# Optimization experiments

Hardware: AMD Instinct MI355X
Metric: run time of the kernel (lower is better)

The kernel has to match this reference:

```python
import jax, jax.numpy as jnp
import numpy as np

EMB = 1024
HEADS = 16
HD = EMB // HEADS

def setup_inputs() -> dict:
    key = jax.random.key(0)
    ks = jax.random.split(key, 9)
    s = 1.0 / np.sqrt(EMB)
    x = jax.random.normal(ks[0], (4, 2048, EMB), dtype=jnp.float32)
    Wq = jax.random.uniform(ks[1], (EMB, EMB), jnp.float32, -s, s)
    bq = jax.random.uniform(ks[2], (EMB,), jnp.float32, -s, s)
    Wk = jax.random.uniform(ks[3], (EMB, EMB), jnp.float32, -s, s)
    bk = jax.random.uniform(ks[4], (EMB,), jnp.float32, -s, s)
    Wv = jax.random.uniform(ks[5], (EMB, EMB), jnp.float32, -s, s)
    bv = jax.random.uniform(ks[6], (EMB,), jnp.float32, -s, s)
    Wo = jax.random.uniform(ks[7], (EMB, EMB), jnp.float32, -s, s)
    bo = jax.random.uniform(ks[8], (EMB,), jnp.float32, -s, s)
    return {"x": x, "Wq": Wq, "bq": bq, "Wk": Wk, "bk": bk, "Wv": Wv, "bv": bv, "Wo": Wo, "bo": bo}

def reference(x, Wq, bq, Wk, bk, Wv, bv, Wo, bo):
    B, T, C = x.shape
    # projections (torch Linear: y = x @ W^T + b)
    q = (x @ Wq.T + bq).reshape(B, T, HEADS, HD).transpose(0, 2, 1, 3)  # [B,H,T,hd]
    k = (x @ Wk.T + bk).reshape(B, T, HEADS, HD).transpose(0, 2, 1, 3)
    v = (x @ Wv.T + bv).reshape(B, T, HEADS, HD).transpose(0, 2, 1, 3)
    scores = jnp.einsum('bhqd,bhkd->bhqk', q, k) / jnp.sqrt(jnp.float32(HD))
    weights = jax.nn.softmax(scores, axis=-1)
    attn = jnp.einsum('bhqk,bhkd->bhqd', weights, v)
    out = attn.transpose(0, 2, 1, 3).reshape(B, T, C)
    return out @ Wo.T + bo
```

## Files before the change

### kernel.cpp

```cpp
#include <hip/hip_runtime.h>

#define TSEQ  2048
#define BATCH 4
#define NHEAD 16
#define EMB   1024

typedef __attribute__((ext_vector_type(8))) __bf16 bf16x8;
typedef __attribute__((ext_vector_type(4))) __bf16 bf16x4;
typedef __attribute__((ext_vector_type(4))) float  floatx4;
typedef __attribute__((ext_vector_type(2))) unsigned int uint32x2;
typedef __attribute__((ext_vector_type(4))) unsigned int uint32x4;

__device__ __forceinline__ void gload_lds16(const __bf16* g, __bf16* lds_uniform_base) {
  __builtin_amdgcn_global_load_lds(
      (__attribute__((address_space(1))) void*)(g),
      (__attribute__((address_space(3))) void*)(lds_uniform_base),
      16, 0, 0);
}

__global__ __launch_bounds__(256) void cvt_f32_bf16(
    const float* __restrict__ src, __bf16* __restrict__ dst)
{
  const int gid = (blockIdx.x * 256 + threadIdx.x) * 4;
  const float4 v = *(const float4*)(src + gid);
  dst[gid + 0] = (__bf16)v.x;
  dst[gid + 1] = (__bf16)v.y;
  dst[gid + 2] = (__bf16)v.z;
  dst[gid + 3] = (__bf16)v.w;
}

__global__ __launch_bounds__(256) void cvt_w4(
    const float* __restrict__ s0, const float* __restrict__ s1,
    const float* __restrict__ s2, const float* __restrict__ s3,
    __bf16* __restrict__ d0, __bf16* __restrict__ d1,
    __bf16* __restrict__ d2, __bf16* __restrict__ d3)
{
  const int z = blockIdx.z;
  const float* src = (z == 0) ? s0 : (z == 1) ? s1 : (z == 2) ? s2 : s3;
  __bf16*      dst = (z == 0) ? d0 : (z == 1) ? d1 : (z == 2) ? d2 : d3;
  const int gid = (blockIdx.x * 256 + threadIdx.x) * 4;
  const float4 v = *(const float4*)(src + gid);
  dst[gid + 0] = (__bf16)v.x;
  dst[gid + 1] = (__bf16)v.y;
  dst[gid + 2] = (__bf16)v.z;
  dst[gid + 3] = (__bf16)v.w;
}

#define GK_NT 16

#define GEMM_STAGE(BUF, K0)                                                               \
  {                                                                                       \
    _Pragma("unroll")                                                                     \
    for (int c = 0; c < 4; c++) {                                                         \
      gload_lds16(aStage + (size_t)(c * 32) * 1024 + (K0),                                \
                  &As[BUF][(c * 32 + wid * 8) * 64]);                                     \
      gload_lds16(bStage + (size_t)(c * 32) * 1024 + (K0),                                \
                  &Bs[BUF][(c * 32 + wid * 8) * 64]);                                     \
    }                                                                                     \
  }

#define GEMM_BODY(C_STORE)                                                                \
  const int tid  = threadIdx.x;                                                           \
  const int lane = tid & 63;                                                              \
  const int wid  = tid >> 6;                                                              \
  const int l16  = lane & 15;                                                             \
  const int quad = lane >> 4;                                                             \
  const int wm   = wid & 1;                                                               \
  const int wn   = wid >> 1;                                                              \
  const int lin = blockIdx.x + blockIdx.y * 8;                                            \
  const int swz = (lin & 7) * 64 + (lin >> 3);                                            \
  const int m0  = (swz >> 3) * 128;                                                       \
  const int n0  = (swz & 7) * 128;                                                        \
  __shared__ alignas(16) __bf16 As[2][128 * 64];                                          \
  __shared__ alignas(16) __bf16 Bs[2][128 * 64];                                          \
  floatx4 acc[4][4];                                                                      \
  _Pragma("unroll")                                                                       \
  for (int i = 0; i < 4; i++)                                                             \
    _Pragma("unroll")                                                                     \
    for (int j = 0; j < 4; j++) acc[i][j] = (floatx4){0.f, 0.f, 0.f, 0.f};                \
  const int lrow = lane >> 3;                                                             \
  const int xsg  = (lane & 7) ^ lrow;                                                     \
  const __bf16* aStage = A + (size_t)(m0 + wid * 8 + lrow) * 1024 + xsg * 8;              \
  const __bf16* bStage = W + (size_t)(n0 + wid * 8 + lrow) * 1024 + xsg * 8;              \
  const int h7 = l16 & 7;                                                                 \
  GEMM_STAGE(0, 0)                                                                        \
  GEMM_STAGE(1, 64)                                                                       \
  __asm__ __volatile__("s_waitcnt vmcnt(8)\n\ts_barrier" ::: "memory");                   \
  int cur = 0;                                                                            \
  _Pragma("unroll 1")                                                                     \
  for (int k = 0; k < GK_NT; ++k) {                                                       \
    bf16x8 af0[4], af1[4], bf0[4], bf1[4];                                                \
    _Pragma("unroll")                                                                     \
    for (int i = 0; i < 4; i++) {                                                         \
      const int ar = (wm * 64 + i * 16 + l16) * 64;                                       \
      const int br = (wn * 64 + i * 16 + l16) * 64;                                       \
      af0[i] = *(const bf16x8*)(&As[cur][ar + ((quad ^ h7)) * 8]);                        \
      af1[i] = *(const bf16x8*)(&As[cur][ar + (((4 + quad) ^ h7)) * 8]);                  \
      bf0[i] = *(const bf16x8*)(&Bs[cur][br + ((quad ^ h7)) * 8]);                        \
      bf1[i] = *(const bf16x8*)(&Bs[cur][br + (((4 + quad) ^ h7)) * 8]);                  \
    }                                                                                     \
    _Pragma("unroll")                                                                     \
    for (int i = 0; i < 4; i++)                                                           \
      _Pragma("unroll")                                                                   \
      for (int j = 0; j < 4; j++) {                                                       \
        acc[i][j] = __builtin_amdgcn_mfma_f32_16x16x32_bf16(af0[i], bf0[j], acc[i][j], 0, 0, 0); \
        acc[i][j] = __builtin_amdgcn_mfma_f32_16x16x32_bf16(af1[i], bf1[j], acc[i][j], 0, 0, 0); \
      }                                                                                   \
    __asm__ __volatile__("s_waitcnt lgkmcnt(0)\n\ts_barrier" ::: "memory");               \
    if (k < GK_NT - 2) {                                                                  \
      GEMM_STAGE(cur, (k + 2) * 64)                                                       \
      __asm__ __volatile__("s_waitcnt vmcnt(8)\n\ts_barrier" ::: "memory");               \
    } else if (k == GK_NT - 2) {                                                          \
      __asm__ __volatile__("s_waitcnt vmcnt(0)\n\ts_barrier" ::: "memory");               \
    }                                                                                     \
    cur ^= 1;                                                                             \
  }                                                                                       \
  float bv[4];                                                                            \
  _Pragma("unroll")                                                                       \
  for (int j = 0; j < 4; j++) bv[j] = Bb[n0 + wn * 64 + j * 16 + l16];                    \
  _Pragma("unroll")                                                                       \
  for (int i = 0; i < 4; i++) {                                                           \
    const size_t mrow = (size_t)m0 + wm * 64 + i * 16 + quad * 4;                         \
    _Pragma("unroll")                                                                     \
    for (int j = 0; j < 4; j++) {                                                         \
      const int col = n0 + wn * 64 + j * 16 + l16;                                        \
      _Pragma("unroll")                                                                   \
      for (int r = 0; r < 4; r++) C_STORE;                                                \
    }                                                                                     \
  }

__global__ __launch_bounds__(256) void gemm_bt_bias(
    const __bf16* __restrict__ A,
    const __bf16* __restrict__ W0, const __bf16* __restrict__ W1, const __bf16* __restrict__ W2,
    const float* __restrict__ B0, const float* __restrict__ B1, const float* __restrict__ B2,
    __bf16* __restrict__ C0, __bf16* __restrict__ C1, __bf16* __restrict__ C2)
{
  const int z = blockIdx.z;
  const __bf16* W  = (z == 0) ? W0 : ((z == 1) ? W1 : W2);
  const float*  Bb = (z == 0) ? B0 : ((z == 1) ? B1 : B2);
  __bf16*       C  = (z == 0) ? C0 : ((z == 1) ? C1 : C2);
  const float  scl = (z == 0) ? 0.125f * 1.44269504088896340736f : 1.0f;
  GEMM_BODY(C[(mrow + r) * 1024 + col] = (__bf16)((acc[i][j][r] + bv[j]) * scl))
}

__global__ __launch_bounds__(256) void gemm_bt_bias_f32(
    const __bf16* __restrict__ A, const __bf16* __restrict__ W,
    const float* __restrict__ Bb, float* __restrict__ C)
{
  GEMM_BODY(C[(mrow + r) * 1024 + col] = acc[i][j][r] + bv[j])
}

__global__ __launch_bounds__(256) void v_transpose(
    const __bf16* __restrict__ V, __bf16* __restrict__ VT)
{
  const int t0 = blockIdx.x * 64;
  const int bh = blockIdx.y;
  const int b  = bh >> 4;
  const int h  = bh & 15;
  const int tid = threadIdx.x;

  __shared__ alignas(16) __bf16 Ls[64 * 72];

  const int row = tid >> 2, seg = tid & 3;
  const __bf16* src = V + ((size_t)(b * TSEQ + t0 + row)) * EMB + h * 64;
  *(bf16x8*)(&Ls[row * 72 + seg * 8])       = *(const bf16x8*)(src + seg * 8);
  *(bf16x8*)(&Ls[row * 72 + (seg + 4) * 8]) = *(const bf16x8*)(src + (seg + 4) * 8);
  __syncthreads();

  const int od = tid >> 2, oseg = tid & 3;
  bf16x8 o0, o1;
#pragma unroll
  for (int j = 0; j < 8; j++) o0[j] = Ls[(oseg * 16 + j) * 72 + od];
#pragma unroll
  for (int j = 0; j < 8; j++) o1[j] = Ls[(oseg * 16 + 8 + j) * 72 + od];
  __bf16* dst = VT + ((size_t)bh * 64 + od) * TSEQ + t0 + oseg * 16;
  *(bf16x8*)(dst)     = o0;
  *(bf16x8*)(dst + 8) = o1;
}

#define KVB 64
#define NT  (TSEQ / KVB)

#define FA_ZERO (floatx4){0.f, 0.f, 0.f, 0.f}

#define FA_STAGE(BUF, TILE)                                                               \
  if ((TILE) < NT) {                                                                      \
    _Pragma("unroll")                                                                     \
    for (int c = 0; c < 2; c++) {                                                         \
      gload_lds16(kstage + (size_t)((TILE) * KVB + c * 8) * EMB,                          \
                  &Ks[BUF][(wid * 16 + c * 8) * 64]);                                     \
      gload_lds16(vstage + (size_t)(c * 8) * TSEQ + (TILE) * KVB,                         \
                  &VTs[BUF][(wid * 16 + c * 8) * 64]);                                    \
    }                                                                                     \
  }

#define SM_PACK(TA, TB, DST)                                                              \
  {                                                                                       \
    bf16x4 pa_, pb_;                                                                      \
    _Pragma("unroll")                                                                     \
    for (int r = 0; r < 4; r++) pa_[r] = (__bf16)__builtin_amdgcn_exp2f((TA)[r]);         \
    _Pragma("unroll")                                                                     \
    for (int r = 0; r < 4; r++) pb_[r] = (__bf16)__builtin_amdgcn_exp2f((TB)[r]);         \
    const uint32x2 A2_ = __builtin_bit_cast(uint32x2, pa_);                               \
    const uint32x2 B2_ = __builtin_bit_cast(uint32x2, pb_);                               \
    const uint32x2 r0_ = __builtin_amdgcn_permlane32_swap(A2_.x, B2_.x, false, false);    \
    const uint32x2 r1_ = __builtin_amdgcn_permlane32_swap(A2_.y, B2_.y, false, false);    \
    const uint32x2 s0_ = __builtin_amdgcn_permlane16_swap(r0_.x, r0_.y, false, false);    \
    const uint32x2 s1_ = __builtin_amdgcn_permlane16_swap(r1_.x, r1_.y, false, false);    \
    const uint32x4 fw_ = (uint32x4){s0_.x, s1_.x, s0_.y, s1_.y};                          \
    DST = __builtin_bit_cast(bf16x8, fw_);                                                \
  }

#define QK_BLOCK(BUF, KS, TA, TB)                                                         \
  {                                                                                       \
    const bf16x8 ka0 = *(const bf16x8*)(&Ks[BUF][(KS) * 2048 + aoff0]);                   \
    const bf16x8 ka1 = *(const bf16x8*)(&Ks[BUF][(KS) * 2048 + aoff1]);                   \
    const bf16x8 kb0 = *(const bf16x8*)(&Ks[BUF][(KS) * 2048 + 1024 + aoff0]);            \
    const bf16x8 kb1 = *(const bf16x8*)(&Ks[BUF][(KS) * 2048 + 1024 + aoff1]);            \
    _Pragma("unroll")                                                                     \
    for (int g = 0; g < 2; g++) {                                                         \
      TA[g] = FA_ZERO;                                                                    \
      TA[g] = __builtin_amdgcn_mfma_f32_16x16x32_bf16(ka0, qf[g][0], TA[g], 0, 0, 0);     \
      TA[g] = __builtin_amdgcn_mfma_f32_16x16x32_bf16(ka1, qf[g][1], TA[g], 0, 0, 0);     \
      TB[g] = FA_ZERO;                                                                    \
      TB[g] = __builtin_amdgcn_mfma_f32_16x16x32_bf16(kb0, qf[g][0], TB[g], 0, 0, 0);     \
      TB[g] = __builtin_amdgcn_mfma_f32_16x16x32_bf16(kb1, qf[g][1], TB[g], 0, 0, 0);     \
    }                                                                                     \
  }

#define FA_STEP(BUF, KT)                                                                  \
  {                                                                                       \
    __builtin_amdgcn_s_setprio(1);                                                        \
    floatx4 ta[2], tb[2];                                                                 \
    QK_BLOCK(BUF, 0, ta, tb)                                                              \
    _Pragma("unroll")                                                                     \
    for (int g = 0; g < 2; g++) {                                                         \
      bf16x8 nf;                                                                          \
      SM_PACK(ta[g], tb[g], nf)                                                           \
      _Pragma("unroll")                                                                   \
      for (int dg = 0; dg < 4; dg++) {                                                    \
        const bf16x8 v0 = *(const bf16x8*)(&VTs[(BUF) ^ 1][dg * 1024 + aoff0]);           \
        Oacc[g][dg] = __builtin_amdgcn_mfma_f32_16x16x32_bf16(v0, pfragP[g][0], Oacc[g][dg], 0, 0, 0); \
      }                                                                                   \
      lacc[g] = __builtin_amdgcn_mfma_f32_16x16x32_bf16(ones, pfragP[g][0], lacc[g], 0, 0, 0); \
      _Pragma("unroll")                                                                   \
      for (int dg = 0; dg < 4; dg++) {                                                    \
        const bf16x8 v1 = *(const bf16x8*)(&VTs[(BUF) ^ 1][dg * 1024 + aoff1]);           \
        Oacc[g][dg] = __builtin_amdgcn_mfma_f32_16x16x32_bf16(v1, pfragP[g][1], Oacc[g][dg], 0, 0, 0); \
      }                                                                                   \
      lacc[g] = __builtin_amdgcn_mfma_f32_16x16x32_bf16(ones, pfragP[g][1], lacc[g], 0, 0, 0); \
      pfragP[g][0] = nf;                                                                  \
    }                                                                                     \
    QK_BLOCK(BUF, 1, ta, tb)                                                              \
    __builtin_amdgcn_s_setprio(0);                                                        \
    __syncthreads();                                                                      \
    FA_STAGE((BUF) ^ 1, (KT) + 1);                                                        \
    _Pragma("unroll")                                                                     \
    for (int g = 0; g < 2; g++) { SM_PACK(ta[g], tb[g], pfragP[g][1]) }                   \
    __syncthreads();                                                                      \
  }

__global__ __launch_bounds__(256, 2) void flash_attn(
    const __bf16* __restrict__ Q, const __bf16* __restrict__ K,
    const __bf16* __restrict__ VT, __bf16* __restrict__ O)
{
  const int lin = blockIdx.x + blockIdx.y * 16;
  const int swz = (lin & 7) * 128 + (lin >> 3);
  const int qt  = swz & 15;
  const int bh  = swz >> 4;
  const int b    = bh >> 4;
  const int h    = bh & 15;
  const int tid  = threadIdx.x;
  const int wid  = tid >> 6;
  const int lane = tid & 63;
  const int l16  = lane & 15;
  const int quad = lane >> 4;

  __shared__ alignas(16) __bf16 Ks[2][KVB * 64];
  __shared__ alignas(16) __bf16 VTs[2][64 * 64];

  const size_t base = ((size_t)b * TSEQ) * EMB + (size_t)h * 64;
  const __bf16* qptr  = Q + base;
  const __bf16* kptr  = K + base;
  const __bf16* vtptr = VT + (size_t)bh * 64 * TSEQ;
  __bf16*       optr  = O + base;

  const int qb = qt * 128 + wid * 32;

  bf16x8 qf[2][2];
#pragma unroll
  for (int g = 0; g < 2; g++)
#pragma unroll
    for (int hf = 0; hf < 2; hf++)
      qf[g][hf] = *(const bf16x8*)(qptr + (size_t)(qb + g * 16 + l16) * EMB + hf * 32 + quad * 8);

  floatx4 Oacc[2][4];
#pragma unroll
  for (int g = 0; g < 2; g++)
#pragma unroll
    for (int dg = 0; dg < 4; dg++) Oacc[g][dg] = FA_ZERO;
  floatx4 lacc[2];
#pragma unroll
  for (int g = 0; g < 2; g++) lacc[g] = FA_ZERO;

  const uint32x4 onesw = (uint32x4){0x3F803F80u, 0x3F803F80u, 0x3F803F80u, 0x3F803F80u};
  const bf16x8 ones = __builtin_bit_cast(bf16x8, onesw);

  const int lrow = lane >> 3;
  const int xsg  = (lane & 7) ^ lrow;
  const __bf16* kstage = kptr  + (size_t)(wid * 16 + lrow) * EMB  + xsg * 8;
  const __bf16* vstage = vtptr + (size_t)(wid * 16 + lrow) * TSEQ + xsg * 8;

  const int h7    = l16 & 7;
  const int x0    = quad ^ h7;
  const int aoff0 = l16 * 64 + x0 * 8;
  const int aoff1 = l16 * 64 + (x0 ^ 4) * 8;

  bf16x8 pfragP[2][2];

  FA_STAGE(0, 0);
  __syncthreads();
  FA_STAGE(1, 1);
  {
    floatx4 ta[2], tb[2];
    QK_BLOCK(0, 0, ta, tb)
#pragma unroll
    for (int g = 0; g < 2; g++) { SM_PACK(ta[g], tb[g], pfragP[g][0]) }
    QK_BLOCK(0, 1, ta, tb)
#pragma unroll
    for (int g = 0; g < 2; g++) { SM_PACK(ta[g], tb[g], pfragP[g][1]) }
  }
  __syncthreads();

#pragma unroll 1
  for (int kt = 1; kt < NT - 1; kt += 2) {
    FA_STEP(1, kt);
    FA_STEP(0, kt + 1);
  }
  FA_STEP(1, NT - 1);

#pragma unroll
  for (int g = 0; g < 2; g++) {
#pragma unroll
    for (int dg = 0; dg < 4; dg++) {
      const bf16x8 v0 = *(const bf16x8*)(&VTs[1][dg * 1024 + aoff0]);
      const bf16x8 v1 = *(const bf16x8*)(&VTs[1][dg * 1024 + aoff1]);
      Oacc[g][dg] = __builtin_amdgcn_mfma_f32_16x16x32_bf16(v0, pfragP[g][0], Oacc[g][dg], 0, 0, 0);
      Oacc[g][dg] = __builtin_amdgcn_mfma_f32_16x16x32_bf16(v1, pfragP[g][1], Oacc[g][dg], 0, 0, 0);
    }
    lacc[g] = __builtin_amdgcn_mfma_f32_16x16x32_bf16(ones, pfragP[g][0], lacc[g], 0, 0, 0);
    lacc[g] = __builtin_amdgcn_mfma_f32_16x16x32_bf16(ones, pfragP[g][1], lacc[g], 0, 0, 0);
  }

#pragma unroll
  for (int g = 0; g < 2; g++) {
    const float inv = 1.0f / lacc[g][0];
#pragma unroll
    for (int dg = 0; dg < 4; dg++) {
      bf16x4 ov;
#pragma unroll
      for (int r = 0; r < 4; r++) ov[r] = (__bf16)(Oacc[g][dg][r] * inv);
      *(bf16x4*)(optr + (size_t)(qb + g * 16 + l16) * EMB + dg * 16 + quad * 4) = ov;
    }
  }
}

extern "C" void kernel_launch(void* const* d_in, const int* in_sizes, int n_in,
                              void* d_out, int out_size, void* d_ws, size_t ws_size,
                              hipStream_t stream) {
  const float* x  = (const float*)d_in[0];
  const float* Wq = (const float*)d_in[1];
  const float* bq = (const float*)d_in[2];
  const float* Wk = (const float*)d_in[3];
  const float* bk = (const float*)d_in[4];
  const float* Wv = (const float*)d_in[5];
  const float* bv = (const float*)d_in[6];
  const float* Wo = (const float*)d_in[7];
  const float* bo = (const float*)d_in[8];
  float* out = (float*)d_out;

  const size_t NELEM = (size_t)BATCH * TSEQ * EMB;
  const size_t WELEM = (size_t)EMB * EMB;

  __bf16* q_b  = (__bf16*)d_out;
  __bf16* k_b  = q_b + NELEM;
  __bf16* x_b  = (__bf16*)d_ws;
  __bf16* v_b  = x_b + NELEM;
  __bf16* wq_b = v_b + NELEM;
  __bf16* wk_b = wq_b + WELEM;
  __bf16* wv_b = wk_b + WELEM;
  __bf16* wo_b = wv_b + WELEM;

  dim3 blk(256, 1, 1);

  cvt_f32_bf16<<<(int)(NELEM / 1024), blk, 0, stream>>>(x, x_b);
  cvt_w4<<<dim3((int)(WELEM / 1024), 1, 4), blk, 0, stream>>>(
      Wq, Wk, Wv, Wo, wq_b, wk_b, wv_b, wo_b);

  gemm_bt_bias<<<dim3(8, 64, 3), blk, 0, stream>>>(
      x_b, wq_b, wk_b, wv_b, bq, bk, bv, q_b, k_b, v_b);

  v_transpose<<<dim3(TSEQ / 64, BATCH * NHEAD), blk, 0, stream>>>(v_b, x_b);

  flash_attn<<<dim3(TSEQ / 128, BATCH * NHEAD), blk, 0, stream>>>(
      q_b, k_b, x_b, v_b);

  gemm_bt_bias_f32<<<dim3(8, 64, 1), blk, 0, stream>>>(v_b, wo_b, bo, out);
}
```

Measured before the change: 265.9 us.

## Enlarge GEMM tiles to 256x128 with 8 waves and double flash-attn query tile

The projection GEMMs move to 512-thread blocks computing 256x128 output tiles. Fragment loads and MFMAs are interleaved in four quadrant phases, with setprio around the MFMAs and barriers between phases, and the next-stage prefetch is issued mid-iteration. Flash attention now processes 256 query rows per block (64 per wave) and hoists the V fragment loads out of the per-group loop, so each K/V tile is reused across more queries. This is meant to cut global/LDS traffic per FLOP and improve MFMA issue density, at the cost of higher register pressure and fewer blocks in the grid.

```diff
diff --git a/kernel.cpp b/kernel.cpp
--- a/kernel.cpp
+++ b/kernel.cpp
@@ -46,32 +46,40 @@
   dst[gid + 3] = (__bf16)v.w;
 }
 
-#define GK_NT 16
-
-#define GEMM_STAGE(BUF, K0)                                                               \
+#define GQ_NT 16
+
+#define G2_STAGE(BUF, T)                                                                  \
   {                                                                                       \
     _Pragma("unroll")                                                                     \
-    for (int c = 0; c < 4; c++) {                                                         \
-      gload_lds16(aStage + (size_t)(c * 32) * 1024 + (K0),                                \
-                  &As[BUF][(c * 32 + wid * 8) * 64]);                                     \
-      gload_lds16(bStage + (size_t)(c * 32) * 1024 + (K0),                                \
-                  &Bs[BUF][(c * 32 + wid * 8) * 64]);                                     \
-    }                                                                                     \
-  }
-
-#define GEMM_BODY(C_STORE)                                                                \
+    for (int c = 0; c < 4; c++)                                                           \
+      gload_lds16(aStage + (size_t)(c * 64) * 1024 + (T) * 64,                            \
+                  &As[BUF][(c * 64 + wid * 8) * 64]);                                     \
+    _Pragma("unroll")                                                                     \
+    for (int c = 0; c < 2; c++)                                                           \
+      gload_lds16(bStage + (size_t)(c * 64) * 1024 + (T) * 64,                            \
+                  &Bs[BUF][(c * 64 + wid * 8) * 64]);                                     \
+  }
+
+#define G2_AF(I, H) (*(const bf16x8*)(&As[cur][(wm * 64 + (I) * 16 + l16) * 64 + (((H) * 4 + quad) ^ h7) * 8]))
+#define G2_BF(J, H) (*(const bf16x8*)(&Bs[cur][(wn * 64 + (J) * 16 + l16) * 64 + (((H) * 4 + quad) ^ h7) * 8]))
+
+#define G2_MFMA_PAIR(I, J)                                                                \
+  acc[I][J] = __builtin_amdgcn_mfma_f32_16x16x32_bf16(af[I][0], bfr[J][0], acc[I][J], 0, 0, 0); \
+  acc[I][J] = __builtin_amdgcn_mfma_f32_16x16x32_bf16(af[I][1], bfr[J][1], acc[I][J], 0, 0, 0);
+
+#define GEMM2_BODY(C_STORE)                                                               \
   const int tid  = threadIdx.x;                                                           \
   const int lane = tid & 63;                                                              \
-  const int wid  = tid >> 6;                                                              \
+  const int wid  = tid >> 6;                                                    \
   const int l16  = lane & 15;                                                             \
   const int quad = lane >> 4;                                                             \
-  const int wm   = wid & 1;                                                               \
-  const int wn   = wid >> 1;                                                              \
-  const int lin = blockIdx.x + blockIdx.y * 8;                                            \
-  const int swz = (lin & 7) * 64 + (lin >> 3);                                            \
-  const int m0  = (swz >> 3) * 128;                                                       \
-  const int n0  = (swz & 7) * 128;                                                        \
-  __shared__ alignas(16) __bf16 As[2][128 * 64];                                          \
+  const int wm   = wid >> 1;                                        \
+  const int wn   = wid & 1;                                         \
+  const int lin  = blockIdx.x + blockIdx.y * 8;                                           \
+  const int swz  = (lin & 7) * 32 + (lin >> 3);                                           \
+  const int m0   = (swz >> 3) * 256;                                                      \
+  const int n0   = (swz & 7) * 128;                                                       \
+  __shared__ alignas(16) __bf16 As[2][256 * 64];                                          \
   __shared__ alignas(16) __bf16 Bs[2][128 * 64];                                          \
   floatx4 acc[4][4];                                                                      \
   _Pragma("unroll")                                                                       \
@@ -83,34 +91,45 @@
   const __bf16* aStage = A + (size_t)(m0 + wid * 8 + lrow) * 1024 + xsg * 8;              \
   const __bf16* bStage = W + (size_t)(n0 + wid * 8 + lrow) * 1024 + xsg * 8;              \
   const int h7 = l16 & 7;                                                                 \
-  GEMM_STAGE(0, 0)                                                                        \
-  GEMM_STAGE(1, 64)                                                                       \
-  __asm__ __volatile__("s_waitcnt vmcnt(8)\n\ts_barrier" ::: "memory");                   \
+  G2_STAGE(0, 0)                                                                          \
+  G2_STAGE(1, 1)                                                                          \
+  __asm__ __volatile__("s_waitcnt vmcnt(6)\n\ts_barrier" ::: "memory");                   \
   int cur = 0;                                                                            \
   _Pragma("unroll 1")                                                                     \
-  for (int k = 0; k < GK_NT; ++k) {                                                       \
-    bf16x8 af0[4], af1[4], bf0[4], bf1[4];                                                \
-    _Pragma("unroll")                                                                     \
-    for (int i = 0; i < 4; i++) {                                                         \
-      const int ar = (wm * 64 + i * 16 + l16) * 64;                                       \
-      const int br = (wn * 64 + i * 16 + l16) * 64;                                       \
-      af0[i] = *(const bf16x8*)(&As[cur][ar + ((quad ^ h7)) * 8]);                        \
-      af1[i] = *(const bf16x8*)(&As[cur][ar + (((4 + quad) ^ h7)) * 8]);                  \
-      bf0[i] = *(const bf16x8*)(&Bs[cur][br + ((quad ^ h7)) * 8]);                        \
-      bf1[i] = *(const bf16x8*)(&Bs[cur][br + (((4 + quad) ^ h7)) * 8]);                  \
-    }                                                                                     \
-    _Pragma("unroll")                                                                     \
-    for (int i = 0; i < 4; i++)                                                           \
-      _Pragma("unroll")                                                                   \
-      for (int j = 0; j < 4; j++) {                                                       \
-        acc[i][j] = __builtin_amdgcn_mfma_f32_16x16x32_bf16(af0[i], bf0[j], acc[i][j], 0, 0, 0); \
-        acc[i][j] = __builtin_amdgcn_mfma_f32_16x16x32_bf16(af1[i], bf1[j], acc[i][j], 0, 0, 0); \
-      }                                                                                   \
-    __asm__ __volatile__("s_waitcnt lgkmcnt(0)\n\ts_barrier" ::: "memory");               \
-    if (k < GK_NT - 2) {                                                                  \
-      GEMM_STAGE(cur, (k + 2) * 64)                                                       \
-      __asm__ __volatile__("s_waitcnt vmcnt(8)\n\ts_barrier" ::: "memory");               \
-    } else if (k == GK_NT - 2) {                                                          \
+  for (int t = 0; t < GQ_NT; ++t) {                                                       \
+    bf16x8 af[4][2], bfr[4][2];                                                           \
+                                    \
+    af[0][0] = G2_AF(0, 0);  af[0][1] = G2_AF(0, 1);                                      \
+    af[1][0] = G2_AF(1, 0);  af[1][1] = G2_AF(1, 1);                                      \
+    bfr[0][0] = G2_BF(0, 0); bfr[0][1] = G2_BF(0, 1);                                     \
+    bfr[1][0] = G2_BF(1, 0); bfr[1][1] = G2_BF(1, 1);                                     \
+    __builtin_amdgcn_s_setprio(1);                                                        \
+    G2_MFMA_PAIR(0, 0) G2_MFMA_PAIR(0, 1) G2_MFMA_PAIR(1, 0) G2_MFMA_PAIR(1, 1)          \
+    __builtin_amdgcn_s_setprio(0);                                                        \
+    __asm__ __volatile__("s_barrier" ::: "memory");                                       \
+                           \
+    bfr[2][0] = G2_BF(2, 0); bfr[2][1] = G2_BF(2, 1);                                     \
+    bfr[3][0] = G2_BF(3, 0); bfr[3][1] = G2_BF(3, 1);                                     \
+    __builtin_amdgcn_s_setprio(1);                                                        \
+    G2_MFMA_PAIR(0, 2) G2_MFMA_PAIR(0, 3) G2_MFMA_PAIR(1, 2) G2_MFMA_PAIR(1, 3)          \
+    __builtin_amdgcn_s_setprio(0);                                                        \
+    __asm__ __volatile__("s_barrier" ::: "memory");                                       \
+                           \
+    af[2][0] = G2_AF(2, 0);  af[2][1] = G2_AF(2, 1);                                      \
+    af[3][0] = G2_AF(3, 0);  af[3][1] = G2_AF(3, 1);                                      \
+    __builtin_amdgcn_s_setprio(1);                                                        \
+    G2_MFMA_PAIR(2, 0) G2_MFMA_PAIR(2, 1) G2_MFMA_PAIR(3, 0) G2_MFMA_PAIR(3, 1)          \
+    __builtin_amdgcn_s_setprio(0);                                                        \
+    __asm__ __volatile__("s_barrier" ::: "memory");                                       \
+                 \
+                 \
+    if (t + 2 < GQ_NT) { G2_STAGE(cur, t + 2) }                                           \
+    __builtin_amdgcn_s_setprio(1);                                                        \
+    G2_MFMA_PAIR(2, 2) G2_MFMA_PAIR(2, 3) G2_MFMA_PAIR(3, 2) G2_MFMA_PAIR(3, 3)          \
+    __builtin_amdgcn_s_setprio(0);                                                        \
+    if (t + 2 < GQ_NT) {                                                                  \
+      __asm__ __volatile__("s_waitcnt vmcnt(6)\n\ts_barrier" ::: "memory");               \
+    } else if (t + 1 < GQ_NT) {                                                           \
       __asm__ __volatile__("s_waitcnt vmcnt(0)\n\ts_barrier" ::: "memory");               \
     }                                                                                     \
     cur ^= 1;                                                                             \
@@ -129,7 +148,7 @@
     }                                                                                     \
   }
 
-__global__ __launch_bounds__(256) void gemm_bt_bias(
+__global__ __launch_bounds__(512, 2) void gemm_bt_bias(
     const __bf16* __restrict__ A,
     const __bf16* __restrict__ W0, const __bf16* __restrict__ W1, const __bf16* __restrict__ W2,
     const float* __restrict__ B0, const float* __restrict__ B1, const float* __restrict__ B2,
@@ -140,14 +159,14 @@
   const float*  Bb = (z == 0) ? B0 : ((z == 1) ? B1 : B2);
   __bf16*       C  = (z == 0) ? C0 : ((z == 1) ? C1 : C2);
   const float  scl = (z == 0) ? 0.125f * 1.44269504088896340736f : 1.0f;
-  GEMM_BODY(C[(mrow + r) * 1024 + col] = (__bf16)((acc[i][j][r] + bv[j]) * scl))
-}
-
-__global__ __launch_bounds__(256) void gemm_bt_bias_f32(
+  GEMM2_BODY(C[(mrow + r) * 1024 + col] = (__bf16)((acc[i][j][r] + bv[j]) * scl))
+}
+
+__global__ __launch_bounds__(512, 2) void gemm_bt_bias_f32(
     const __bf16* __restrict__ A, const __bf16* __restrict__ W,
     const float* __restrict__ Bb, float* __restrict__ C)
 {
-  GEMM_BODY(C[(mrow + r) * 1024 + col] = acc[i][j][r] + bv[j])
+  GEMM2_BODY(C[(mrow + r) * 1024 + col] = acc[i][j][r] + bv[j])
 }
 
 __global__ __launch_bounds__(256) void v_transpose(
@@ -218,7 +237,7 @@
     const bf16x8 kb0 = *(const bf16x8*)(&Ks[BUF][(KS) * 2048 + 1024 + aoff0]);            \
     const bf16x8 kb1 = *(const bf16x8*)(&Ks[BUF][(KS) * 2048 + 1024 + aoff1]);            \
     _Pragma("unroll")                                                                     \
-    for (int g = 0; g < 2; g++) {                                                         \
+    for (int g = 0; g < 4; g++) {                                                         \
       TA[g] = FA_ZERO;                                                                    \
       TA[g] = __builtin_amdgcn_mfma_f32_16x16x32_bf16(ka0, qf[g][0], TA[g], 0, 0, 0);     \
       TA[g] = __builtin_amdgcn_mfma_f32_16x16x32_bf16(ka1, qf[g][1], TA[g], 0, 0, 0);     \
@@ -231,23 +250,25 @@
 #define FA_STEP(BUF, KT)                                                                  \
   {                                                                                       \
     __builtin_amdgcn_s_setprio(1);                                                        \
-    floatx4 ta[2], tb[2];                                                                 \
+    bf16x8 vf[4][2];                                                                      \
+    _Pragma("unroll")                                                                     \
+    for (int dg = 0; dg < 4; dg++) {                                                      \
+      vf[dg][0] = *(const bf16x8*)(&VTs[(BUF) ^ 1][dg * 1024 + aoff0]);                   \
+      vf[dg][1] = *(const bf16x8*)(&VTs[(BUF) ^ 1][dg * 1024 + aoff1]);                   \
+    }                                                                                     \
+    floatx4 ta[4], tb[4];                                                                 \
     QK_BLOCK(BUF, 0, ta, tb)                                                              \
     _Pragma("unroll")                                                                     \
-    for (int g = 0; g < 2; g++) {                                                         \
+    for (int g = 0; g < 4; g++) {                                                         \
       bf16x8 nf;                                                                          \
       SM_PACK(ta[g], tb[g], nf)                                                           \
       _Pragma("unroll")                                                                   \
-      for (int dg = 0; dg < 4; dg++) {                                                    \
-        const bf16x8 v0 = *(const bf16x8*)(&VTs[(BUF) ^ 1][dg * 1024 + aoff0]);           \
-        Oacc[g][dg] = __builtin_amdgcn_mfma_f32_16x16x32_bf16(v0, pfragP[g][0], Oacc[g][dg], 0, 0, 0); \
-      }                                                                                   \
+      for (int dg = 0; dg < 4; dg++)                                                      \
+        Oacc[g][dg] = __builtin_amdgcn_mfma_f32_16x16x32_bf16(vf[dg][0], pfragP[g][0], Oacc[g][dg], 0, 0, 0); \
       lacc[g] = __builtin_amdgcn_mfma_f32_16x16x32_bf16(ones, pfragP[g][0], lacc[g], 0, 0, 0); \
       _Pragma("unroll")                                                                   \
-      for (int dg = 0; dg < 4; dg++) {                                                    \
-        const bf16x8 v1 = *(const bf16x8*)(&VTs[(BUF) ^ 1][dg * 1024 + aoff1]);           \
-        Oacc[g][dg] = __builtin_amdgcn_mfma_f32_16x16x32_bf16(v1, pfragP[g][1], Oacc[g][dg], 0, 0, 0); \
-      }                                                                                   \
+      for (int dg = 0; dg < 4; dg++)                                                      \
+        Oacc[g][dg] = __builtin_amdgcn_mfma_f32_16x16x32_bf16(vf[dg][1], pfragP[g][1], Oacc[g][dg], 0, 0, 0); \
       lacc[g] = __builtin_amdgcn_mfma_f32_16x16x32_bf16(ones, pfragP[g][1], lacc[g], 0, 0, 0); \
       pfragP[g][0] = nf;                                                                  \
     }                                                                                     \
@@ -256,7 +277,7 @@
     __syncthreads();                                                                      \
     FA_STAGE((BUF) ^ 1, (KT) + 1);                                                        \
     _Pragma("unroll")                                                                     \
-    for (int g = 0; g < 2; g++) { SM_PACK(ta[g], tb[g], pfragP[g][1]) }                   \
+    for (int g = 0; g < 4; g++) { SM_PACK(ta[g], tb[g], pfragP[g][1]) }                   \
     __syncthreads();                                                                      \
   }
 
@@ -264,10 +285,10 @@
     const __bf16* __restrict__ Q, const __bf16* __restrict__ K,
     const __bf16* __restrict__ VT, __bf16* __restrict__ O)
 {
-  const int lin = blockIdx.x + blockIdx.y * 16;
-  const int swz = (lin & 7) * 128 + (lin >> 3);
-  const int qt  = swz & 15;
-  const int bh  = swz >> 4;
+  const int lin = blockIdx.x + blockIdx.y * 8;
+  const int swz = (lin & 7) * 64 + (lin >> 3);
+  const int qt  = swz & 7;
+  const int bh  = swz >> 3;
   const int b    = bh >> 4;
   const int h    = bh & 15;
   const int tid  = threadIdx.x;
@@ -285,23 +306,23 @@
   const __bf16* vtptr = VT + (size_t)bh * 64 * TSEQ;
   __bf16*       optr  = O + base;
 
-  const int qb = qt * 128 + wid * 32;
-
-  bf16x8 qf[2][2];
-#pragma unroll
-  for (int g = 0; g < 2; g++)
+  const int qb = qt * 256 + wid * 64;
+
+  bf16x8 qf[4][2];
+#pragma unroll
+  for (int g = 0; g < 4; g++)
 #pragma unroll
     for (int hf = 0; hf < 2; hf++)
       qf[g][hf] = *(const bf16x8*)(qptr + (size_t)(qb + g * 16 + l16) * EMB + hf * 32 + quad * 8);
 
-  floatx4 Oacc[2][4];
-#pragma unroll
-  for (int g = 0; g < 2; g++)
+  floatx4 Oacc[4][4];
+#pragma unroll
+  for (int g = 0; g < 4; g++)
 #pragma unroll
     for (int dg = 0; dg < 4; dg++) Oacc[g][dg] = FA_ZERO;
-  floatx4 lacc[2];
-#pragma unroll
-  for (int g = 0; g < 2; g++) lacc[g] = FA_ZERO;
+  floatx4 lacc[4];
+#pragma unroll
+  for (int g = 0; g < 4; g++) lacc[g] = FA_ZERO;
 
   const uint32x4 onesw = (uint32x4){0x3F803F80u, 0x3F803F80u, 0x3F803F80u, 0x3F803F80u};
   const bf16x8 ones = __builtin_bit_cast(bf16x8, onesw);
@@ -316,19 +337,19 @@
   const int aoff0 = l16 * 64 + x0 * 8;
   const int aoff1 = l16 * 64 + (x0 ^ 4) * 8;
 
-  bf16x8 pfragP[2][2];
+  bf16x8 pfragP[4][2];
 
   FA_STAGE(0, 0);
   __syncthreads();
   FA_STAGE(1, 1);
   {
-    floatx4 ta[2], tb[2];
+    floatx4 ta[4], tb[4];
     QK_BLOCK(0, 0, ta, tb)
 #pragma unroll
-    for (int g = 0; g < 2; g++) { SM_PACK(ta[g], tb[g], pfragP[g][0]) }
+    for (int g = 0; g < 4; g++) { SM_PACK(ta[g], tb[g], pfragP[g][0]) }
     QK_BLOCK(0, 1, ta, tb)
 #pragma unroll
-    for (int g = 0; g < 2; g++) { SM_PACK(ta[g], tb[g], pfragP[g][1]) }
+    for (int g = 0; g < 4; g++) { SM_PACK(ta[g], tb[g], pfragP[g][1]) }
   }
   __syncthreads();
 
@@ -340,7 +361,7 @@
   FA_STEP(1, NT - 1);
 
 #pragma unroll
-  for (int g = 0; g < 2; g++) {
+  for (int g = 0; g < 4; g++) {
 #pragma unroll
     for (int dg = 0; dg < 4; dg++) {
       const bf16x8 v0 = *(const bf16x8*)(&VTs[1][dg * 1024 + aoff0]);
@@ -353,7 +374,7 @@
   }
 
 #pragma unroll
-  for (int g = 0; g < 2; g++) {
+  for (int g = 0; g < 4; g++) {
     const float inv = 1.0f / lacc[g][0];
 #pragma unroll
     for (int dg = 0; dg < 4; dg++) {
@@ -392,18 +413,19 @@
   __bf16* wo_b = wv_b + WELEM;
 
   dim3 blk(256, 1, 1);
+  dim3 blk512(512, 1, 1);
 
   cvt_f32_bf16<<<(int)(NELEM / 1024), blk, 0, stream>>>(x, x_b);
   cvt_w4<<<dim3((int)(WELEM / 1024), 1, 4), blk, 0, stream>>>(
       Wq, Wk, Wv, Wo, wq_b, wk_b, wv_b, wo_b);
 
-  gemm_bt_bias<<<dim3(8, 64, 3), blk, 0, stream>>>(
+  gemm_bt_bias<<<dim3(8, 32, 3), blk512, 0, stream>>>(
       x_b, wq_b, wk_b, wv_b, bq, bk, bv, q_b, k_b, v_b);
 
   v_transpose<<<dim3(TSEQ / 64, BATCH * NHEAD), blk, 0, stream>>>(v_b, x_b);
 
-  flash_attn<<<dim3(TSEQ / 128, BATCH * NHEAD), blk, 0, stream>>>(
+  flash_attn<<<dim3(TSEQ / 256, BATCH * NHEAD), blk, 0, stream>>>(
       q_b, k_b, x_b, v_b);
 
-  gemm_bt_bias_f32<<<dim3(8, 64, 1), blk, 0, stream>>>(v_b, wo_b, bo, out);
-}
+  gemm_bt_bias_f32<<<dim3(8, 32, 1), blk512, 0, stream>>>(v_b, wo_b, bo, out);
+}
```

Measured after the change: 271.7 us. 2.2% more time.
